# Performance work log

Hardware: AMD Instinct MI355X
Metric: run time of the kernel (lower is better)

Reference implementation:

```python
import jax, jax.numpy as jnp
import numpy as np

N_HEADS = 16
HEAD_DIM = 64  # dim=1024 / n_heads=16


def setup_inputs() -> dict:
    key = jax.random.key(0)
    ks = jax.random.split(key, 7)
    B, S, D = 4, 2048, 1024
    scale = 1.0 / np.sqrt(D)
    return {
        "q": jax.random.normal(ks[0], (B, S, D), jnp.float32),
        "k": jax.random.normal(ks[1], (B, S, D), jnp.float32),
        "v": jax.random.normal(ks[2], (B, S, D), jnp.float32),
        "Wq": jax.random.normal(ks[3], (D, D), jnp.float32) * scale,
        "Wk": jax.random.normal(ks[4], (D, D), jnp.float32) * scale,
        "Wv": jax.random.normal(ks[5], (D, D), jnp.float32) * scale,
        "Wo": jax.random.normal(ks[6], (D, D), jnp.float32) * scale,
    }


def reference(q, k, v, Wq, Wk, Wv, Wo):
    B, S, _ = q.shape
    H, Dh = N_HEADS, HEAD_DIM
    # linear projections (torch Linear: x @ W.T), reshape to [B, H, S, Dh]
    xq = (q @ Wq.T).reshape(B, S, H, Dh).transpose(0, 2, 1, 3)
    xk = (k @ Wk.T).reshape(B, S, H, Dh).transpose(0, 2, 1, 3)
    xv = (v @ Wv.T).reshape(B, S, H, Dh).transpose(0, 2, 1, 3)
    scores = jnp.einsum("bhsd,bhtd->bhst", xq, xk) / jnp.sqrt(jnp.float32(Dh))
    # causal mask: -inf above diagonal
    causal = jnp.triu(jnp.full((S, S), -jnp.inf, jnp.float32), k=1)
    scores = scores + causal[None, None]
    attn = jax.nn.softmax(scores.astype(jnp.float32), axis=-1).astype(xq.dtype)
    out = jnp.einsum("bhst,bhtd->bhsd", attn, xv)
    out = out.transpose(0, 2, 1, 3).reshape(B, S, H * Dh)
    return out @ Wo.T
```

## Files before the change

kernel.cpp:

```cpp
#include <hip/hip_runtime.h>
#include <hip/hip_bf16.h>

#define DI __device__ __forceinline__

typedef __attribute__((ext_vector_type(8))) short short8;
typedef __attribute__((ext_vector_type(4))) short short4v;
typedef __attribute__((ext_vector_type(4))) float f32x4;

#define QSCALE 0.180336885f

DI short f2bf(float f) {
  __hip_bfloat16 h = __float2bfloat16(f);
  return __builtin_bit_cast(short, h);
}

DI float fexp2(float x) {
#if __has_builtin(__builtin_amdgcn_exp2f)
  return __builtin_amdgcn_exp2f(x);
#else
  return exp2f(x);
#endif
}

DI void gl16(const short* g, short* l) {
  __builtin_amdgcn_global_load_lds(
      (const __attribute__((address_space(1))) void*)g,
      (__attribute__((address_space(3))) void*)l, 16, 0, 0);
}

__global__ __launch_bounds__(256) void convert_w(
    const float* __restrict__ wq, const float* __restrict__ wk,
    const float* __restrict__ wv, const float* __restrict__ wo,
    short* __restrict__ dst) {
  int z = blockIdx.z;
  const float* src = (z == 0) ? wq : (z == 1) ? wk : (z == 2) ? wv : wo;
  short* d = dst + (size_t)z * 1024 * 1024;
  int i = (blockIdx.x * 256 + threadIdx.x) * 4;
  float4 f = *(const float4*)(src + i);
  short4v v;
  v[0] = f2bf(f.x); v[1] = f2bf(f.y); v[2] = f2bf(f.z); v[3] = f2bf(f.w);
  *(short4v*)(d + i) = v;
}

__global__ __launch_bounds__(256) void convert_x(
    const float* __restrict__ q, const float* __restrict__ k,
    const float* __restrict__ v, short* __restrict__ qb,
    short* __restrict__ kb, short* __restrict__ vb) {
  int z = blockIdx.z;
  const float* src = (z == 0) ? q : (z == 1) ? k : v;
  short* dst = (z == 0) ? qb : (z == 1) ? kb : vb;
  size_t i = ((size_t)blockIdx.x * 256 + threadIdx.x) * 8;
  float4 f0 = *(const float4*)(src + i);
  float4 f1 = *(const float4*)(src + i + 4);
  short8 o;
  o[0] = f2bf(f0.x); o[1] = f2bf(f0.y); o[2] = f2bf(f0.z); o[3] = f2bf(f0.w);
  o[4] = f2bf(f1.x); o[5] = f2bf(f1.y); o[6] = f2bf(f1.z); o[7] = f2bf(f1.w);
  *(short8*)(dst + i) = o;
}

__global__ __launch_bounds__(256) void convert_one(
    const float* __restrict__ src, short* __restrict__ dst) {
  size_t i = ((size_t)blockIdx.x * 256 + threadIdx.x) * 8;
  float4 f0 = *(const float4*)(src + i);
  float4 f1 = *(const float4*)(src + i + 4);
  short8 o;
  o[0] = f2bf(f0.x); o[1] = f2bf(f0.y); o[2] = f2bf(f0.z); o[3] = f2bf(f0.w);
  o[4] = f2bf(f1.x); o[5] = f2bf(f1.y); o[6] = f2bf(f1.z); o[7] = f2bf(f1.w);
  *(short8*)(dst + i) = o;
}

enum { OUT_F32 = 0, OUT_HEAD = 1, OUT_HEADT = 2 };

template <int OMODE>
DI void gemm_core(short* sA, short* sB, const short* __restrict__ A,
                  const short* __restrict__ B, void* __restrict__ Cp,
                  float scale, int bm, int bn) {
  const int tid = threadIdx.x;
  const int lane = tid & 63;
  const int wid = tid >> 6;
  const int wm = wid >> 1, wn = wid & 1;
  const int l15 = lane & 15, lq = lane >> 4;
  const int lrr = lane >> 3;
  const int lch = lane & 7;

  f32x4 acc[4][4] = {};

  for (int k0 = 0; k0 < 1024; k0 += 64) {
#pragma unroll
    for (int i = 0; i < 4; ++i) {
      int r0 = wid * 32 + i * 8;
      int rr = r0 + lrr;
      int sc = (lch ^ (rr & 7)) << 3;
      gl16(A + (size_t)(bm + rr) * 1024 + k0 + sc, sA + r0 * 64);
      gl16(B + (size_t)(bn + rr) * 1024 + k0 + sc, sB + r0 * 64);
    }
    __syncthreads();

#pragma unroll
    for (int ks = 0; ks < 2; ++ks) {
      short8 a[4], b[4];
#pragma unroll
      for (int mt = 0; mt < 4; ++mt) {
        int row = wm * 64 + mt * 16 + l15;
        int off = (row * 128 + ks * 64 + lq * 16) ^ ((row & 7) << 4);
        a[mt] = *(const short8*)((const char*)sA + off);
      }
#pragma unroll
      for (int nt = 0; nt < 4; ++nt) {
        int row = wn * 64 + nt * 16 + l15;
        int off = (row * 128 + ks * 64 + lq * 16) ^ ((row & 7) << 4);
        b[nt] = *(const short8*)((const char*)sB + off);
      }
#pragma unroll
      for (int mt = 0; mt < 4; ++mt)
#pragma unroll
        for (int nt = 0; nt < 4; ++nt) {
          if (OMODE == OUT_HEADT)
            acc[mt][nt] = __builtin_amdgcn_mfma_f32_16x16x32_bf16(
                b[nt], a[mt], acc[mt][nt], 0, 0, 0);
          else
            acc[mt][nt] = __builtin_amdgcn_mfma_f32_16x16x32_bf16(
                a[mt], b[nt], acc[mt][nt], 0, 0, 0);
        }
    }
    __syncthreads();
  }

#pragma unroll
  for (int mt = 0; mt < 4; ++mt) {
#pragma unroll
    for (int nt = 0; nt < 4; ++nt) {
#pragma unroll
      for (int r = 0; r < 4; ++r) {
        float val = acc[mt][nt][r] * scale;
        if (OMODE == OUT_HEADT) {
          int f = bn + wn * 64 + nt * 16 + lq * 4 + r;
          int t = bm + wm * 64 + mt * 16 + l15;
          int bb = t >> 11, s = t & 2047;
          int h = f >> 6, dh = f & 63;
          ((short*)Cp)[((size_t)((bb * 16 + h) * 64 + dh)) * 2048 + s] = f2bf(val);
        } else {
          int rowg = bm + wm * 64 + mt * 16 + lq * 4 + r;
          int colg = bn + wn * 64 + nt * 16 + l15;
          if (OMODE == OUT_HEAD) {
            int bb = rowg >> 11, s = rowg & 2047;
            int h = colg >> 6, dh = colg & 63;
            ((short*)Cp)[((size_t)(bb * 16 + h) * 2048 + s) * 64 + dh] = f2bf(val);
          } else {
            ((float*)Cp)[(size_t)rowg * 1024 + colg] = val;
          }
        }
      }
    }
  }
}

DI void xcd_map(int id, int& bm, int& bn) {
  int xcd = id & 7, slot = id >> 3;
  int panel = xcd + 8 * (slot >> 3);
  int ntile = slot & 7;
  bm = panel * 128;
  bn = ntile * 128;
}

#define GEMM_LDS()                              \
  __shared__ __align__(16) short sA[128 * 64];  \
  __shared__ __align__(16) short sB[128 * 64];

__global__ __launch_bounds__(256) void proj_gemm3(
    const short* __restrict__ qb, const short* __restrict__ kb,
    const short* __restrict__ vb, const short* __restrict__ wq,
    const short* __restrict__ wk, const short* __restrict__ wv,
    short* __restrict__ xq, short* __restrict__ xk, short* __restrict__ xvT) {
  GEMM_LDS();
  int z = blockIdx.z;
  int bm, bn;
  xcd_map(blockIdx.x, bm, bn);
  if (z == 0) {
    gemm_core<OUT_HEAD>(sA, sB, qb, wq, xq, QSCALE, bm, bn);
  } else if (z == 1) {
    gemm_core<OUT_HEAD>(sA, sB, kb, wk, xk, 1.0f, bm, bn);
  } else {
    gemm_core<OUT_HEADT>(sA, sB, vb, wv, xvT, 1.0f, bm, bn);
  }
}

__global__ __launch_bounds__(256) void proj_oneN(
    const short* __restrict__ A, const short* __restrict__ B,
    short* __restrict__ C, float scale) {
  GEMM_LDS();
  int bm, bn;
  xcd_map(blockIdx.x, bm, bn);
  gemm_core<OUT_HEAD>(sA, sB, A, B, C, scale, bm, bn);
}

__global__ __launch_bounds__(256) void proj_oneT(
    const short* __restrict__ A, const short* __restrict__ B,
    short* __restrict__ C, float scale) {
  GEMM_LDS();
  int bm, bn;
  xcd_map(blockIdx.x, bm, bn);
  gemm_core<OUT_HEADT>(sA, sB, A, B, C, scale, bm, bn);
}

__global__ __launch_bounds__(256) void final_gemm(
    const short* __restrict__ oa, const short* __restrict__ wo,
    float* __restrict__ out) {
  GEMM_LDS();
  int bm, bn;
  xcd_map(blockIdx.x, bm, bn);
  gemm_core<OUT_F32>(sA, sB, oa, wo, out, 1.0f, bm, bn);
}

__global__ __launch_bounds__(512, 4) void attn_k(
    const short* __restrict__ Xq, const short* __restrict__ Xk,
    const short* __restrict__ XvT, short* __restrict__ Oa) {
  __shared__ __align__(16) short sK[2][64 * 64];
  __shared__ __align__(16) short sVT[2][64 * 64];
  __shared__ __align__(16) short sP[8][16 * 64];

  const int tid = threadIdx.x;
  const int lane = tid & 63;
  const int wid = tid >> 6;
  const int l15 = lane & 15, lq = lane >> 4;
  const int bid = blockIdx.x;
  const int ipair = bid >> 6;
  const int bh = bid & 63;
  const int b = bh >> 4, h = bh & 15;

  const short* Q = Xq + (size_t)bh * 2048 * 64;
  const short* K = Xk + (size_t)bh * 2048 * 64;
  const short* VT = XvT + (size_t)bh * 64 * 2048;

  const int srow = tid >> 3;
  const int scol = (tid & 7) * 8;
  const int soff = (srow * 128 + scol * 2) ^ ((srow & 7) << 4);

  short8 kreg, vreg;
  kreg = *(const short8*)(K + (size_t)srow * 64 + scol);
  vreg = *(const short8*)(VT + (size_t)srow * 2048 + scol);

  *(short8*)((char*)sK[0] + soff) = kreg;
  *(short8*)((char*)sVT[0] + soff) = vreg;

  short* sPw = sP[wid];
  int p = 0;

  for (int seg = 0; seg < 2; ++seg) {
    const int qt = seg ? ipair : (15 - ipair);
    const int qfirst = qt * 128 + wid * 16;
    const int qg = qfirst + l15;
    const int qlast = qfirst + 15;
    const int ntile = 2 * qt + 2;

    short8 qf[2];
#pragma unroll
    for (int ks = 0; ks < 2; ++ks)
      qf[ks] = *(const short8*)(Q + (size_t)qg * 64 + ks * 32 + lq * 8);

    float m_run = -1e30f, l_run = 0.f;
    f32x4 acc[4] = {};

    for (int kt = 0; kt < ntile; ++kt) {
      const int kv0 = kt * 64;
      __syncthreads();

      int nkt = kt + 1, nseg = seg;
      if (nkt >= ntile) { nseg = seg + 1; nkt = 0; }
      const bool hn = (nseg < 2);
      if (hn) {
        const int kn = nkt * 64;
        kreg = *(const short8*)(K + (size_t)(kn + srow) * 64 + scol);
        vreg = *(const short8*)(VT + (size_t)srow * 2048 + kn + scol);
      }

      const bool fullmask = (kv0 > qlast);
      if (!fullmask) {
        const bool needmask = (kv0 + 63 > qfirst);
        const char* bufK = (const char*)sK[p];
        const char* bufV = (const char*)sVT[p];

        f32x4 sc[4] = {};
        __builtin_amdgcn_s_setprio(1);
#pragma unroll
        for (int ks = 0; ks < 2; ++ks) {
          short8 kf[4];
#pragma unroll
          for (int nt = 0; nt < 4; ++nt) {
            int row = nt * 16 + l15;
            int off = (row * 128 + ks * 64 + lq * 16) ^ ((row & 7) << 4);
            kf[nt] = *(const short8*)(bufK + off);
          }
#pragma unroll
          for (int nt = 0; nt < 4; ++nt)
            sc[nt] = __builtin_amdgcn_mfma_f32_16x16x32_bf16(kf[nt], qf[ks],
                                                             sc[nt], 0, 0, 0);
        }
        __builtin_amdgcn_s_setprio(0);

        float pv[4][4];
        float m = -1e30f;
        if (needmask) {
#pragma unroll
          for (int nt = 0; nt < 4; ++nt)
#pragma unroll
            for (int r = 0; r < 4; ++r) {
              float s = sc[nt][r];
              if (kv0 + nt * 16 + lq * 4 + r > qg) s = -1e30f;
              pv[nt][r] = s;
              m = fmaxf(m, s);
            }
        } else {
#pragma unroll
          for (int nt = 0; nt < 4; ++nt)
#pragma unroll
            for (int r = 0; r < 4; ++r) {
              float s = sc[nt][r];
              pv[nt][r] = s;
              m = fmaxf(m, s);
            }
        }
        m = fmaxf(m, __shfl_xor(m, 16));
        m = fmaxf(m, __shfl_xor(m, 32));

        if (!__all(m - m_run <= 8.0f)) {
          const float m_new = fmaxf(m_run, m);
          const float corr = fexp2(m_run - m_new);
          l_run *= corr;
#pragma unroll
          for (int mt = 0; mt < 4; ++mt)
#pragma unroll
            for (int r = 0; r < 4; ++r) acc[mt][r] *= corr;
          m_run = m_new;
        }

        float rsum = 0.f;
#pragma unroll
        for (int nt = 0; nt < 4; ++nt)
#pragma unroll
          for (int r = 0; r < 4; ++r) {
            float e = fexp2(pv[nt][r] - m_run);
            pv[nt][r] = e;
            rsum += e;
          }
        rsum += __shfl_xor(rsum, 16);
        rsum += __shfl_xor(rsum, 32);
        l_run += rsum;

#pragma unroll
        for (int nt = 0; nt < 4; ++nt) {
          short4v pw;
#pragma unroll
          for (int r = 0; r < 4; ++r) pw[r] = f2bf(pv[nt][r]);
          int off = (l15 * 128 + nt * 32 + lq * 8) ^ ((l15 & 7) << 4);
          *(short4v*)((char*)sPw + off) = pw;
        }

        __builtin_amdgcn_s_setprio(1);
#pragma unroll
        for (int ks = 0; ks < 2; ++ks) {
          int poff = (l15 * 128 + ks * 64 + lq * 16) ^ ((l15 & 7) << 4);
          short8 pf = *(const short8*)((const char*)sPw + poff);
#pragma unroll
          for (int mt = 0; mt < 4; ++mt) {
            int row = mt * 16 + l15;
            int voff = (row * 128 + ks * 64 + lq * 16) ^ ((row & 7) << 4);
            short8 vf = *(const short8*)(bufV + voff);
            acc[mt] = __builtin_amdgcn_mfma_f32_16x16x32_bf16(vf, pf, acc[mt],
                                                              0, 0, 0);
          }
        }
        __builtin_amdgcn_s_setprio(0);
      }

      if (hn) {
        *(short8*)((char*)sK[p ^ 1] + soff) = kreg;
        *(short8*)((char*)sVT[p ^ 1] + soff) = vreg;
      }
      p ^= 1;
    }

    const float rl = 1.0f / l_run;
    short* orow = Oa + ((size_t)(b * 2048 + qg)) * 1024 + h * 64;
#pragma unroll
    for (int mt = 0; mt < 4; ++mt) {
      short4v o;
#pragma unroll
      for (int r = 0; r < 4; ++r) o[r] = f2bf(acc[mt][r] * rl);
      *(short4v*)(orow + mt * 16 + lq * 4) = o;
    }
  }
}

extern "C" void kernel_launch(void* const* d_in, const int* in_sizes, int n_in,
                              void* d_out, int out_size, void* d_ws,
                              size_t ws_size, hipStream_t stream) {
  const float* q = (const float*)d_in[0];
  const float* k = (const float*)d_in[1];
  const float* v = (const float*)d_in[2];
  const float* Wq = (const float*)d_in[3];
  const float* Wk = (const float*)d_in[4];
  const float* Wv = (const float*)d_in[5];
  const float* Wo = (const float*)d_in[6];

  char* ws = (char*)d_ws;
  short* wq_b = (short*)(ws + (0ull << 20));
  short* wk_b = (short*)(ws + (2ull << 20));
  short* wv_b = (short*)(ws + (4ull << 20));
  short* wo_b = (short*)(ws + (6ull << 20));
  short* xq  = (short*)(ws + (8ull << 20));
  short* xk  = (short*)(ws + (24ull << 20));
  short* xvT = (short*)(ws + (56ull << 20));

  convert_w<<<dim3(1024, 1, 4), 256, 0, stream>>>(Wq, Wk, Wv, Wo, wq_b);

  if (ws_size >= (122ull << 20)) {
    short* qb = (short*)(ws + (72ull << 20));
    short* kb = (short*)(ws + (88ull << 20));
    short* vb = (short*)(ws + (104ull << 20));
    short* oa = qb;

    convert_x<<<dim3(4096, 1, 3), 256, 0, stream>>>(q, k, v, qb, kb, vb);
    proj_gemm3<<<dim3(512, 1, 3), 256, 0, stream>>>(qb, kb, vb, wq_b, wk_b,
                                                    wv_b, xq, xk, xvT);
    attn_k<<<dim3(512), 512, 0, stream>>>(xq, xk, xvT, oa);
    final_gemm<<<dim3(512), 256, 0, stream>>>(oa, wo_b, (float*)d_out);
  } else {
    short* X = (short*)(ws + (8ull << 20));
    short* xq2 = (short*)(ws + (24ull << 20));
    short* xk2 = (short*)(ws + (40ull << 20));
    short* xvT2 = (short*)(ws + (56ull << 20));
    short* oa2 = (short*)(ws + (72ull << 20));

    convert_one<<<dim3(4096), 256, 0, stream>>>(q, X);
    proj_oneN<<<dim3(512), 256, 0, stream>>>(X, wq_b, xq2, QSCALE);
    convert_one<<<dim3(4096), 256, 0, stream>>>(k, X);
    proj_oneN<<<dim3(512), 256, 0, stream>>>(X, wk_b, xk2, 1.0f);
    convert_one<<<dim3(4096), 256, 0, stream>>>(v, X);
    proj_oneT<<<dim3(512), 256, 0, stream>>>(X, wv_b, xvT2, 1.0f);
    attn_k<<<dim3(512), 512, 0, stream>>>(xq2, xk2, xvT2, oa2);
    final_gemm<<<dim3(512), 256, 0, stream>>>(oa2, wo_b, (float*)d_out);
  }
}
```

Baseline: 177.1 us.

## Process two 16-row query groups per wave in attention with 256-thread blocks

The attention kernel now runs 4 waves per block instead of 8, and each wave handles two 16-row query groups that sit 64 rows apart. Each K fragment read from LDS feeds the MFMAs for both groups, and each V fragment feeds both PV MFMAs, which halves LDS fragment traffic per query row. The causal masking logic is simplified to tile-index checks. The cost is higher register pressure from doubled accumulators and Q fragments, fewer waves per block, and a dropped occupancy hint in the launch bounds.

```diff
diff --git a/kernel.cpp b/kernel.cpp
--- a/kernel.cpp
+++ b/kernel.cpp
@@ -212,12 +212,12 @@
   gemm_core<OUT_F32>(sA, sB, oa, wo, out, 1.0f, bm, bn);
 }
 
-__global__ __launch_bounds__(512, 4) void attn_k(
+__global__ __launch_bounds__(256) void attn_k(
     const short* __restrict__ Xq, const short* __restrict__ Xk,
     const short* __restrict__ XvT, short* __restrict__ Oa) {
   __shared__ __align__(16) short sK[2][64 * 64];
   __shared__ __align__(16) short sVT[2][64 * 64];
-  __shared__ __align__(16) short sP[8][16 * 64];
+  __shared__ __align__(16) short sP[4][2][16 * 64];
 
   const int tid = threadIdx.x;
   const int lane = tid & 63;
@@ -234,32 +234,41 @@
 
   const int srow = tid >> 3;
   const int scol = (tid & 7) * 8;
-  const int soff = (srow * 128 + scol * 2) ^ ((srow & 7) << 4);
-
-  short8 kreg, vreg;
-  kreg = *(const short8*)(K + (size_t)srow * 64 + scol);
-  vreg = *(const short8*)(VT + (size_t)srow * 2048 + scol);
-
-  *(short8*)((char*)sK[0] + soff) = kreg;
-  *(short8*)((char*)sVT[0] + soff) = vreg;
-
-  short* sPw = sP[wid];
+  const int soff0 = (srow * 128 + scol * 2) ^ ((srow & 7) << 4);
+  const int soff1 = ((srow + 32) * 128 + scol * 2) ^ ((srow & 7) << 4);
+
+  short8 kreg[2], vreg[2];
+  kreg[0] = *(const short8*)(K + (size_t)srow * 64 + scol);
+  kreg[1] = *(const short8*)(K + (size_t)(srow + 32) * 64 + scol);
+  vreg[0] = *(const short8*)(VT + (size_t)srow * 2048 + scol);
+  vreg[1] = *(const short8*)(VT + (size_t)(srow + 32) * 2048 + scol);
+
+  *(short8*)((char*)sK[0] + soff0) = kreg[0];
+  *(short8*)((char*)sK[0] + soff1) = kreg[1];
+  *(short8*)((char*)sVT[0] + soff0) = vreg[0];
+  *(short8*)((char*)sVT[0] + soff1) = vreg[1];
+
+  short* sPw0 = sP[wid][0];
+  short* sPw1 = sP[wid][1];
   int p = 0;
 
   for (int seg = 0; seg < 2; ++seg) {
     const int qt = seg ? ipair : (15 - ipair);
-    const int qfirst = qt * 128 + wid * 16;
-    const int qg = qfirst + l15;
-    const int qlast = qfirst + 15;
+    const int g0first = qt * 128 + wid * 16;
+    const int g1first = g0first + 64;
+    const int qg0 = g0first + l15;
+    const int qg1 = g1first + l15;
     const int ntile = 2 * qt + 2;
 
-    short8 qf[2];
-#pragma unroll
-    for (int ks = 0; ks < 2; ++ks)
-      qf[ks] = *(const short8*)(Q + (size_t)qg * 64 + ks * 32 + lq * 8);
-
-    float m_run = -1e30f, l_run = 0.f;
-    f32x4 acc[4] = {};
+    short8 qf0[2], qf1[2];
+#pragma unroll
+    for (int ks = 0; ks < 2; ++ks) {
+      qf0[ks] = *(const short8*)(Q + (size_t)qg0 * 64 + ks * 32 + lq * 8);
+      qf1[ks] = *(const short8*)(Q + (size_t)qg1 * 64 + ks * 32 + lq * 8);
+    }
+
+    float m0 = -1e30f, l0 = 0.f, m1 = -1e30f, l1 = 0.f;
+    f32x4 acc0[4] = {}, acc1[4] = {};
 
     for (int kt = 0; kt < ntile; ++kt) {
       const int kv0 = kt * 64;
@@ -270,43 +279,52 @@
       const bool hn = (nseg < 2);
       if (hn) {
         const int kn = nkt * 64;
-        kreg = *(const short8*)(K + (size_t)(kn + srow) * 64 + scol);
-        vreg = *(const short8*)(VT + (size_t)srow * 2048 + kn + scol);
-      }
-
-      const bool fullmask = (kv0 > qlast);
-      if (!fullmask) {
-        const bool needmask = (kv0 + 63 > qfirst);
-        const char* bufK = (const char*)sK[p];
-        const char* bufV = (const char*)sVT[p];
-
-        f32x4 sc[4] = {};
-        __builtin_amdgcn_s_setprio(1);
-#pragma unroll
-        for (int ks = 0; ks < 2; ++ks) {
-          short8 kf[4];
-#pragma unroll
-          for (int nt = 0; nt < 4; ++nt) {
-            int row = nt * 16 + l15;
-            int off = (row * 128 + ks * 64 + lq * 16) ^ ((row & 7) << 4);
-            kf[nt] = *(const short8*)(bufK + off);
-          }
+        kreg[0] = *(const short8*)(K + (size_t)(kn + srow) * 64 + scol);
+        kreg[1] = *(const short8*)(K + (size_t)(kn + srow + 32) * 64 + scol);
+        vreg[0] = *(const short8*)(VT + (size_t)srow * 2048 + kn + scol);
+        vreg[1] = *(const short8*)(VT + (size_t)(srow + 32) * 2048 + kn + scol);
+      }
+
+      const bool g0a = (kt < ntile - 1);
+      const bool mask0 = (kt == ntile - 2);
+      const bool mask1 = (kt == ntile - 1);
+      const char* bufK = (const char*)sK[p];
+      const char* bufV = (const char*)sVT[p];
+
+      f32x4 sc0[4] = {}, sc1[4] = {};
+      __builtin_amdgcn_s_setprio(1);
+#pragma unroll
+      for (int ks = 0; ks < 2; ++ks) {
+        short8 kf[4];
+#pragma unroll
+        for (int nt = 0; nt < 4; ++nt) {
+          int row = nt * 16 + l15;
+          int off = (row * 128 + ks * 64 + lq * 16) ^ ((row & 7) << 4);
+          kf[nt] = *(const short8*)(bufK + off);
+        }
+#pragma unroll
+        for (int nt = 0; nt < 4; ++nt)
+          sc1[nt] = __builtin_amdgcn_mfma_f32_16x16x32_bf16(kf[nt], qf1[ks],
+                                                            sc1[nt], 0, 0, 0);
+        if (g0a) {
 #pragma unroll
           for (int nt = 0; nt < 4; ++nt)
-            sc[nt] = __builtin_amdgcn_mfma_f32_16x16x32_bf16(kf[nt], qf[ks],
-                                                             sc[nt], 0, 0, 0);
-        }
-        __builtin_amdgcn_s_setprio(0);
-
+            sc0[nt] = __builtin_amdgcn_mfma_f32_16x16x32_bf16(kf[nt], qf0[ks],
+                                                              sc0[nt], 0, 0, 0);
+        }
+      }
+      __builtin_amdgcn_s_setprio(0);
+
+      {
         float pv[4][4];
         float m = -1e30f;
-        if (needmask) {
+        if (mask1) {
 #pragma unroll
           for (int nt = 0; nt < 4; ++nt)
 #pragma unroll
             for (int r = 0; r < 4; ++r) {
-              float s = sc[nt][r];
-              if (kv0 + nt * 16 + lq * 4 + r > qg) s = -1e30f;
+              float s = sc1[nt][r];
+              if (kv0 + nt * 16 + lq * 4 + r > qg1) s = -1e30f;
               pv[nt][r] = s;
               m = fmaxf(m, s);
             }
@@ -315,79 +333,146 @@
           for (int nt = 0; nt < 4; ++nt)
 #pragma unroll
             for (int r = 0; r < 4; ++r) {
-              float s = sc[nt][r];
+              float s = sc1[nt][r];
               pv[nt][r] = s;
               m = fmaxf(m, s);
             }
         }
         m = fmaxf(m, __shfl_xor(m, 16));
         m = fmaxf(m, __shfl_xor(m, 32));
-
-        if (!__all(m - m_run <= 8.0f)) {
-          const float m_new = fmaxf(m_run, m);
-          const float corr = fexp2(m_run - m_new);
-          l_run *= corr;
+        if (!__all(m - m1 <= 8.0f)) {
+          const float mn = fmaxf(m1, m);
+          const float corr = fexp2(m1 - mn);
+          l1 *= corr;
 #pragma unroll
           for (int mt = 0; mt < 4; ++mt)
 #pragma unroll
-            for (int r = 0; r < 4; ++r) acc[mt][r] *= corr;
-          m_run = m_new;
-        }
-
-        float rsum = 0.f;
+            for (int r = 0; r < 4; ++r) acc1[mt][r] *= corr;
+          m1 = mn;
+        }
+        float rs = 0.f;
 #pragma unroll
         for (int nt = 0; nt < 4; ++nt)
 #pragma unroll
           for (int r = 0; r < 4; ++r) {
-            float e = fexp2(pv[nt][r] - m_run);
+            float e = fexp2(pv[nt][r] - m1);
             pv[nt][r] = e;
-            rsum += e;
+            rs += e;
           }
-        rsum += __shfl_xor(rsum, 16);
-        rsum += __shfl_xor(rsum, 32);
-        l_run += rsum;
-
+        rs += __shfl_xor(rs, 16);
+        rs += __shfl_xor(rs, 32);
+        l1 += rs;
 #pragma unroll
         for (int nt = 0; nt < 4; ++nt) {
           short4v pw;
 #pragma unroll
           for (int r = 0; r < 4; ++r) pw[r] = f2bf(pv[nt][r]);
           int off = (l15 * 128 + nt * 32 + lq * 8) ^ ((l15 & 7) << 4);
-          *(short4v*)((char*)sPw + off) = pw;
-        }
-
-        __builtin_amdgcn_s_setprio(1);
-#pragma unroll
-        for (int ks = 0; ks < 2; ++ks) {
-          int poff = (l15 * 128 + ks * 64 + lq * 16) ^ ((l15 & 7) << 4);
-          short8 pf = *(const short8*)((const char*)sPw + poff);
-#pragma unroll
-          for (int mt = 0; mt < 4; ++mt) {
-            int row = mt * 16 + l15;
-            int voff = (row * 128 + ks * 64 + lq * 16) ^ ((row & 7) << 4);
-            short8 vf = *(const short8*)(bufV + voff);
-            acc[mt] = __builtin_amdgcn_mfma_f32_16x16x32_bf16(vf, pf, acc[mt],
-                                                              0, 0, 0);
+          *(short4v*)((char*)sPw1 + off) = pw;
+        }
+      }
+
+      if (g0a) {
+        float pv[4][4];
+        float m = -1e30f;
+        if (mask0) {
+#pragma unroll
+          for (int nt = 0; nt < 4; ++nt)
+#pragma unroll
+            for (int r = 0; r < 4; ++r) {
+              float s = sc0[nt][r];
+              if (kv0 + nt * 16 + lq * 4 + r > qg0) s = -1e30f;
+              pv[nt][r] = s;
+              m = fmaxf(m, s);
+            }
+        } else {
+#pragma unroll
+          for (int nt = 0; nt < 4; ++nt)
+#pragma unroll
+            for (int r = 0; r < 4; ++r) {
+              float s = sc0[nt][r];
+              pv[nt][r] = s;
+              m = fmaxf(m, s);
+            }
+        }
+        m = fmaxf(m, __shfl_xor(m, 16));
+        m = fmaxf(m, __shfl_xor(m, 32));
+        if (!__all(m - m0 <= 8.0f)) {
+          const float mn = fmaxf(m0, m);
+          const float corr = fexp2(m0 - mn);
+          l0 *= corr;
+#pragma unroll
+          for (int mt = 0; mt < 4; ++mt)
+#pragma unroll
+            for (int r = 0; r < 4; ++r) acc0[mt][r] *= corr;
+          m0 = mn;
+        }
+        float rs = 0.f;
+#pragma unroll
+        for (int nt = 0; nt < 4; ++nt)
+#pragma unroll
+          for (int r = 0; r < 4; ++r) {
+            float e = fexp2(pv[nt][r] - m0);
+            pv[nt][r] = e;
+            rs += e;
           }
-        }
-        __builtin_amdgcn_s_setprio(0);
-      }
+        rs += __shfl_xor(rs, 16);
+        rs += __shfl_xor(rs, 32);
+        l0 += rs;
+#pragma unroll
+        for (int nt = 0; nt < 4; ++nt) {
+          short4v pw;
+#pragma unroll
+          for (int r = 0; r < 4; ++r) pw[r] = f2bf(pv[nt][r]);
+          int off = (l15 * 128 + nt * 32 + lq * 8) ^ ((l15 & 7) << 4);
+          *(short4v*)((char*)sPw0 + off) = pw;
+        }
+      }
+
+      __builtin_amdgcn_s_setprio(1);
+#pragma unroll
+      for (int ks = 0; ks < 2; ++ks) {
+        int poff = (l15 * 128 + ks * 64 + lq * 16) ^ ((l15 & 7) << 4);
+        short8 pf1 = *(const short8*)((const char*)sPw1 + poff);
+        short8 pf0;
+        if (g0a) pf0 = *(const short8*)((const char*)sPw0 + poff);
+#pragma unroll
+        for (int mt = 0; mt < 4; ++mt) {
+          int row = mt * 16 + l15;
+          int voff = (row * 128 + ks * 64 + lq * 16) ^ ((row & 7) << 4);
+          short8 vf = *(const short8*)(bufV + voff);
+          acc1[mt] = __builtin_amdgcn_mfma_f32_16x16x32_bf16(vf, pf1, acc1[mt],
+                                                             0, 0, 0);
+          if (g0a)
+            acc0[mt] = __builtin_amdgcn_mfma_f32_16x16x32_bf16(vf, pf0,
+                                                               acc0[mt], 0, 0, 0);
+        }
+      }
+      __builtin_amdgcn_s_setprio(0);
 
       if (hn) {
-        *(short8*)((char*)sK[p ^ 1] + soff) = kreg;
-        *(short8*)((char*)sVT[p ^ 1] + soff) = vreg;
+        *(short8*)((char*)sK[p ^ 1] + soff0) = kreg[0];
+        *(short8*)((char*)sK[p ^ 1] + soff1) = kreg[1];
+        *(short8*)((char*)sVT[p ^ 1] + soff0) = vreg[0];
+        *(short8*)((char*)sVT[p ^ 1] + soff1) = vreg[1];
       }
       p ^= 1;
     }
 
-    const float rl = 1.0f / l_run;
-    short* orow = Oa + ((size_t)(b * 2048 + qg)) * 1024 + h * 64;
+    const float rl0 = 1.0f / l0;
+    const float rl1 = 1.0f / l1;
+    short* orow0 = Oa + ((size_t)(b * 2048 + qg0)) * 1024 + h * 64;
+    short* orow1 = Oa + ((size_t)(b * 2048 + qg1)) * 1024 + h * 64;
 #pragma unroll
     for (int mt = 0; mt < 4; ++mt) {
-      short4v o;
-#pragma unroll
-      for (int r = 0; r < 4; ++r) o[r] = f2bf(acc[mt][r] * rl);
-      *(short4v*)(orow + mt * 16 + lq * 4) = o;
+      short4v o0, o1;
+#pragma unroll
+      for (int r = 0; r < 4; ++r) {
+        o0[r] = f2bf(acc0[mt][r] * rl0);
+        o1[r] = f2bf(acc1[mt][r] * rl1);
+      }
+      *(short4v*)(orow0 + mt * 16 + lq * 4) = o0;
+      *(short4v*)(orow1 + mt * 16 + lq * 4) = o1;
     }
   }
 }
@@ -423,7 +508,7 @@
     convert_x<<<dim3(4096, 1, 3), 256, 0, stream>>>(q, k, v, qb, kb, vb);
     proj_gemm3<<<dim3(512, 1, 3), 256, 0, stream>>>(qb, kb, vb, wq_b, wk_b,
                                                     wv_b, xq, xk, xvT);
-    attn_k<<<dim3(512), 512, 0, stream>>>(xq, xk, xvT, oa);
+    attn_k<<<dim3(512), 256, 0, stream>>>(xq, xk, xvT, oa);
     final_gemm<<<dim3(512), 256, 0, stream>>>(oa, wo_b, (float*)d_out);
   } else {
     short* X = (short*)(ws + (8ull << 20));
@@ -438,7 +523,7 @@
     proj_oneN<<<dim3(512), 256, 0, stream>>>(X, wk_b, xk2, 1.0f);
     convert_one<<<dim3(4096), 256, 0, stream>>>(v, X);
     proj_oneT<<<dim3(512), 256, 0, stream>>>(X, wv_b, xvT2, 1.0f);
-    attn_k<<<dim3(512), 512, 0, stream>>>(xq2, xk2, xvT2, oa2);
+    attn_k<<<dim3(512), 256, 0, stream>>>(xq2, xk2, xvT2, oa2);
     final_gemm<<<dim3(512), 256, 0, stream>>>(oa2, wo_b, (float*)d_out);
   }
 }
```

Result: slower. 270.9 us (+53.0%).

## Double-buffer GEMM LDS tiles and merge input/weight conversion into one launch

Applied to the files above, without the earlier changes.

The shared GEMM core now uses two LDS buffers per operand. It issues the global-to-LDS loads for the next k-tile before running the MFMAs on the current one, so memory latency can overlap with compute and one barrier per iteration is removed. The weight and activation fp32-to-bf16 conversions are merged into a single kernel launch, saving one launch on the main path. The trade-off is double the LDS per GEMM block, which may lower occupancy. The merged grid also launches many early-exit blocks for the weight slices, and the fallback path redundantly converts Wq across four z-slices.

```diff
diff --git a/kernel.cpp b/kernel.cpp
--- a/kernel.cpp
+++ b/kernel.cpp
@@ -28,27 +28,23 @@
       (__attribute__((address_space(3))) void*)l, 16, 0, 0);
 }
 
-__global__ __launch_bounds__(256) void convert_w(
-    const float* __restrict__ wq, const float* __restrict__ wk,
-    const float* __restrict__ wv, const float* __restrict__ wo,
-    short* __restrict__ dst) {
+__global__ __launch_bounds__(256) void convert_all(
+    const float* __restrict__ q, const float* __restrict__ k,
+    const float* __restrict__ v, const float* __restrict__ wq,
+    const float* __restrict__ wk, const float* __restrict__ wv,
+    const float* __restrict__ wo, short* __restrict__ qb,
+    short* __restrict__ kb, short* __restrict__ vb, short* __restrict__ wb) {
   int z = blockIdx.z;
-  const float* src = (z == 0) ? wq : (z == 1) ? wk : (z == 2) ? wv : wo;
-  short* d = dst + (size_t)z * 1024 * 1024;
-  int i = (blockIdx.x * 256 + threadIdx.x) * 4;
-  float4 f = *(const float4*)(src + i);
-  short4v v;
-  v[0] = f2bf(f.x); v[1] = f2bf(f.y); v[2] = f2bf(f.z); v[3] = f2bf(f.w);
-  *(short4v*)(d + i) = v;
-}
-
-__global__ __launch_bounds__(256) void convert_x(
-    const float* __restrict__ q, const float* __restrict__ k,
-    const float* __restrict__ v, short* __restrict__ qb,
-    short* __restrict__ kb, short* __restrict__ vb) {
-  int z = blockIdx.z;
-  const float* src = (z == 0) ? q : (z == 1) ? k : v;
-  short* dst = (z == 0) ? qb : (z == 1) ? kb : vb;
+  const float* src;
+  short* dst;
+  if (z < 3) {
+    src = (z == 0) ? q : (z == 1) ? k : v;
+    dst = (z == 0) ? qb : (z == 1) ? kb : vb;
+  } else {
+    if (blockIdx.x >= 512) return;
+    src = (z == 3) ? wq : (z == 4) ? wk : (z == 5) ? wv : wo;
+    dst = wb + (size_t)(z - 3) * 1024 * 1024;
+  }
   size_t i = ((size_t)blockIdx.x * 256 + threadIdx.x) * 8;
   float4 f0 = *(const float4*)(src + i);
   float4 f1 = *(const float4*)(src + i + 4);
@@ -70,6 +66,19 @@
 }
 
 enum { OUT_F32 = 0, OUT_HEAD = 1, OUT_HEADT = 2 };
+
+DI void stage_tile(const short* __restrict__ A, const short* __restrict__ B,
+                   short* dA, short* dB, int bm, int bn, int k0, int wid,
+                   int lrr, int lch) {
+#pragma unroll
+  for (int i = 0; i < 4; ++i) {
+    int r0 = wid * 32 + i * 8;
+    int rr = r0 + lrr;
+    int sc = (lch ^ (rr & 7)) << 3;
+    gl16(A + (size_t)(bm + rr) * 1024 + k0 + sc, dA + r0 * 64);
+    gl16(B + (size_t)(bn + rr) * 1024 + k0 + sc, dB + r0 * 64);
+  }
+}
 
 template <int OMODE>
 DI void gemm_core(short* sA, short* sB, const short* __restrict__ A,
@@ -85,17 +94,17 @@
 
   f32x4 acc[4][4] = {};
 
-  for (int k0 = 0; k0 < 1024; k0 += 64) {
-#pragma unroll
-    for (int i = 0; i < 4; ++i) {
-      int r0 = wid * 32 + i * 8;
-      int rr = r0 + lrr;
-      int sc = (lch ^ (rr & 7)) << 3;
-      gl16(A + (size_t)(bm + rr) * 1024 + k0 + sc, sA + r0 * 64);
-      gl16(B + (size_t)(bn + rr) * 1024 + k0 + sc, sB + r0 * 64);
-    }
-    __syncthreads();
-
+  stage_tile(A, B, sA, sB, bm, bn, 0, wid, lrr, lch);
+  __syncthreads();
+
+  int cur = 0;
+  for (int t = 0; t < 16; ++t) {
+    if (t + 1 < 16)
+      stage_tile(A, B, sA + (cur ^ 1) * 8192, sB + (cur ^ 1) * 8192, bm, bn,
+                 (t + 1) * 64, wid, lrr, lch);
+
+    const char* bA = (const char*)(sA + cur * 8192);
+    const char* bB = (const char*)(sB + cur * 8192);
 #pragma unroll
     for (int ks = 0; ks < 2; ++ks) {
       short8 a[4], b[4];
@@ -103,13 +112,13 @@
       for (int mt = 0; mt < 4; ++mt) {
         int row = wm * 64 + mt * 16 + l15;
         int off = (row * 128 + ks * 64 + lq * 16) ^ ((row & 7) << 4);
-        a[mt] = *(const short8*)((const char*)sA + off);
+        a[mt] = *(const short8*)(bA + off);
       }
 #pragma unroll
       for (int nt = 0; nt < 4; ++nt) {
         int row = wn * 64 + nt * 16 + l15;
         int off = (row * 128 + ks * 64 + lq * 16) ^ ((row & 7) << 4);
-        b[nt] = *(const short8*)((const char*)sB + off);
+        b[nt] = *(const short8*)(bB + off);
       }
 #pragma unroll
       for (int mt = 0; mt < 4; ++mt)
@@ -124,6 +133,7 @@
         }
     }
     __syncthreads();
+    cur ^= 1;
   }
 
 #pragma unroll
@@ -163,9 +173,9 @@
   bn = ntile * 128;
 }
 
-#define GEMM_LDS()                              \
-  __shared__ __align__(16) short sA[128 * 64];  \
-  __shared__ __align__(16) short sB[128 * 64];
+#define GEMM_LDS()                                  \
+  __shared__ __align__(16) short sA[2 * 128 * 64];  \
+  __shared__ __align__(16) short sB[2 * 128 * 64];
 
 __global__ __launch_bounds__(256) void proj_gemm3(
     const short* __restrict__ qb, const short* __restrict__ kb,
@@ -412,15 +422,14 @@
   short* xk  = (short*)(ws + (24ull << 20));
   short* xvT = (short*)(ws + (56ull << 20));
 
-  convert_w<<<dim3(1024, 1, 4), 256, 0, stream>>>(Wq, Wk, Wv, Wo, wq_b);
-
   if (ws_size >= (122ull << 20)) {
     short* qb = (short*)(ws + (72ull << 20));
     short* kb = (short*)(ws + (88ull << 20));
     short* vb = (short*)(ws + (104ull << 20));
     short* oa = qb;
 
-    convert_x<<<dim3(4096, 1, 3), 256, 0, stream>>>(q, k, v, qb, kb, vb);
+    convert_all<<<dim3(4096, 1, 7), 256, 0, stream>>>(q, k, v, Wq, Wk, Wv, Wo,
+                                                      qb, kb, vb, wq_b);
     proj_gemm3<<<dim3(512, 1, 3), 256, 0, stream>>>(qb, kb, vb, wq_b, wk_b,
                                                     wv_b, xq, xk, xvT);
     attn_k<<<dim3(512), 512, 0, stream>>>(xq, xk, xvT, oa);
@@ -432,6 +441,10 @@
     short* xvT2 = (short*)(ws + (56ull << 20));
     short* oa2 = (short*)(ws + (72ull << 20));
 
+    convert_one<<<dim3(512, 1, 4), 256, 0, stream>>>(Wq, wq_b);
+    convert_one<<<dim3(512), 256, 0, stream>>>(Wk, wk_b);
+    convert_one<<<dim3(512), 256, 0, stream>>>(Wv, wv_b);
+    convert_one<<<dim3(512), 256, 0, stream>>>(Wo, wo_b);
     convert_one<<<dim3(4096), 256, 0, stream>>>(q, X);
     proj_oneN<<<dim3(512), 256, 0, stream>>>(X, wq_b, xq2, QSCALE);
     convert_one<<<dim3(4096), 256, 0, stream>>>(k, X);
```

Result: no change. 176.6 us (-0.3%).
